# Kernel tuning notes

Measured on AMD Instinct MI355X. Metric: run time of the kernel, lower is better.

## Reference

```python
import jax, jax.numpy as jnp
import numpy as np

N = 50000          # num nodes
E = 1_000_000      # num edges (no self loops by construction)
IN_CH = 128        # in_channels
HEADS = 4
OUT_CH = 16        # out_channels per head
HID = HEADS * OUT_CH  # 64
NEG_SLOPE = 0.2


def setup_inputs() -> dict:
    key = jax.random.key(0)
    k1, k2, k3, k4, k5, k6 = jax.random.split(key, 6)
    x = jax.random.normal(k1, (N, IN_CH), jnp.float32)
    # edges with guaranteed row != col (so add_self_loops == plain concat)
    row = jax.random.randint(k2, (E,), 0, N, dtype=jnp.int32)
    off = jax.random.randint(k3, (E,), 1, N, dtype=jnp.int32)
    col = (row + off) % N
    edge_index = jnp.stack([row, col], axis=0)  # [2, E]
    # xavier-uniform linear weight [HID, IN_CH] (bias=False in module)
    lim_w = float(np.sqrt(6.0 / (IN_CH + HID)))
    W = jax.random.uniform(k4, (HID, IN_CH), jnp.float32, -lim_w, lim_w)
    # xavier-uniform attention vectors [HEADS, OUT_CH]
    lim_a = float(np.sqrt(6.0 / (HEADS + OUT_CH)))
    att_src = jax.random.uniform(k5, (HEADS, OUT_CH), jnp.float32, -lim_a, lim_a)
    att_dst = jax.random.uniform(k6, (HEADS, OUT_CH), jnp.float32, -lim_a, lim_a)
    bias = jnp.zeros((HID,), jnp.float32)
    return {"x": x, "edge_index": edge_index, "W": W,
            "att_src": att_src, "att_dst": att_dst, "bias": bias}


def reference(x, edge_index, W, att_src, att_dst, bias):
    # add self loops (input edges have no self loops, so this matches torch)
    loops = jnp.arange(N, dtype=edge_index.dtype)
    ei = jnp.concatenate([edge_index, jnp.stack([loops, loops], axis=0)], axis=1)
    row, col = ei[0], ei[1]                      # [E+N]
    proj = (x @ W.T).reshape(N, HEADS, OUT_CH)   # [N, H, C]
    src = proj[row]                              # [E+N, H, C] gather
    dst = proj[col]                              # [E+N, H, C] gather
    # MX attention logits per edge per head
    logits = (jnp.einsum('ehc,hc->eh', src, att_src)
              + jnp.einsum('ehc,hc->eh', dst, att_dst))
    logits = jax.nn.leaky_relu(logits, NEG_SLOPE)            # [E+N, H]
    # segment softmax over destination node (all heads at once)
    m = jax.ops.segment_max(logits, col, num_segments=N)    # [N, H]
    e = jnp.exp(logits - m[col])
    s = jax.ops.segment_sum(e, col, num_segments=N)         # [N, H]
    w = e / s[col]                                           # [E+N, H]
    # attention-weighted scatter-add aggregation
    out = jax.ops.segment_sum(src * w[..., None], col, num_segments=N)  # [N, H, C]
    return out.reshape(N, HID) + bias
```

## Files before the change

kernel.cpp:

```cpp
#include <hip/hip_runtime.h>

#define IN_CH   128
#define HEADS   4
#define OUT_CH  16
#define HID     64
#define NEG_SLOPE 0.2f
#define LOG2E   1.44269504088896340736f

#define LDA 136

#define RB      6
#define RSZ     64
#define NRANGE  1024
#define SEG     8192
#define RWIN    2048

typedef __attribute__((ext_vector_type(8))) short short8;
typedef __attribute__((ext_vector_type(4))) float float4v;

__device__ __forceinline__ unsigned short f2bf(float f) {
    unsigned int u = __float_as_uint(f);
    u += 0x7FFFu + ((u >> 16) & 1u);
    return (unsigned short)(u >> 16);
}
__device__ __forceinline__ unsigned int cvt_pk_bf16(float lo, float hi) {
    unsigned int r;
    asm("v_cvt_pk_bf16_f32 %0, %1, %2" : "=v"(r) : "v"(lo), "v"(hi));
    return r;
}
__device__ __forceinline__ void unpack2(unsigned int u, float& lo, float& hi) {
    lo = __uint_as_float(u << 16);
    hi = __uint_as_float(u & 0xffff0000u);
}

__global__ __launch_bounds__(256) void proj_bin_kernel(
    const float* __restrict__ x,
    const float* __restrict__ W,
    const float* __restrict__ att_src,
    const float* __restrict__ att_dst,
    unsigned short* __restrict__ proj,
    float* __restrict__ asrc,
    float* __restrict__ adst,
    const int* __restrict__ src,
    const int* __restrict__ dst,
    int* __restrict__ gcur,
    unsigned int* __restrict__ ebuf,
    int n_nodes, int n_edges, int nblk_proj)
{
    __shared__ __align__(16) char smraw[SEG * 4 + NRANGE * 4];

    const int tid = threadIdx.x;

    if (blockIdx.x >= nblk_proj) {
        unsigned int* eb = (unsigned int*)smraw;
        int*          lc = (int*)(smraw + SEG * 4);

        const int b = blockIdx.x - nblk_proj;
        #pragma unroll
        for (int i = tid; i < NRANGE; i += 256) lc[i] = 0;
        __syncthreads();

        const int e0  = b * SEG;
        const int e1  = min(e0 + SEG, n_edges);
        const int cnt = e1 - e0;

        for (int e = e0 + tid * 4; e < e1; e += 1024) {
            if (e + 4 <= e1) {
                const int4 s4 = *(const int4*)(src + e);
                const int4 d4 = *(const int4*)(dst + e);
                {
                    const int r = d4.x >> RB; atomicAdd(&lc[r], 1);
                    eb[e - e0 + 0] = ((unsigned int)r << 22) | ((unsigned int)(d4.x & (RSZ - 1)) << 16) | (unsigned int)s4.x;
                }
                {
                    const int r = d4.y >> RB; atomicAdd(&lc[r], 1);
                    eb[e - e0 + 1] = ((unsigned int)r << 22) | ((unsigned int)(d4.y & (RSZ - 1)) << 16) | (unsigned int)s4.y;
                }
                {
                    const int r = d4.z >> RB; atomicAdd(&lc[r], 1);
                    eb[e - e0 + 2] = ((unsigned int)r << 22) | ((unsigned int)(d4.z & (RSZ - 1)) << 16) | (unsigned int)s4.z;
                }
                {
                    const int r = d4.w >> RB; atomicAdd(&lc[r], 1);
                    eb[e - e0 + 3] = ((unsigned int)r << 22) | ((unsigned int)(d4.w & (RSZ - 1)) << 16) | (unsigned int)s4.w;
                }
            } else {
                for (int q = e; q < e1; ++q) {
                    const int d = dst[q];
                    const int r = d >> RB;
                    atomicAdd(&lc[r], 1);
                    eb[q - e0] = ((unsigned int)r << 22) | ((unsigned int)(d & (RSZ - 1)) << 16) | (unsigned int)src[q];
                }
            }
        }
        __syncthreads();

        for (int r = tid; r < NRANGE; r += 256) {
            const int c = lc[r];
            if (c) lc[r] = r * RWIN + atomicAdd(&gcur[r], c);
        }
        __syncthreads();

        for (int j = tid; j < cnt; j += 256) {
            const unsigned int p = eb[j];
            const int slot = atomicAdd(&lc[p >> 22], 1);
            ebuf[slot] = p & 0x3FFFFFu;
        }
        return;
    }

    unsigned short* As = (unsigned short*)smraw;
    unsigned short* Bs = (unsigned short*)(smraw + 64 * LDA * 2);

    const int n0 = blockIdx.x * 64;

    #pragma unroll
    for (int i = 0; i < 8; ++i) {
        int idx4 = i * 256 + tid;
        int row  = idx4 >> 5;
        int c4   = (idx4 & 31) * 4;
        float4 v = *(const float4*)(W + row * IN_CH + c4);
        uint2 o;
        o.x = cvt_pk_bf16(v.x, v.y);
        o.y = cvt_pk_bf16(v.z, v.w);
        *(uint2*)(&Bs[row * LDA + c4]) = o;
    }
    #pragma unroll
    for (int i = 0; i < 8; ++i) {
        int idx4 = i * 256 + tid;
        int row  = idx4 >> 5;
        int c4   = (idx4 & 31) * 4;
        int n    = n0 + row;
        float4 v = make_float4(0.f, 0.f, 0.f, 0.f);
        if (n < n_nodes) v = *(const float4*)(x + (size_t)n * IN_CH + c4);
        uint2 o;
        o.x = cvt_pk_bf16(v.x, v.y);
        o.y = cvt_pk_bf16(v.z, v.w);
        *(uint2*)(&As[row * LDA + c4]) = o;
    }
    __syncthreads();

    const int w    = tid >> 6;
    const int lane = tid & 63;
    const int l16  = lane & 15;
    const int quad = lane >> 4;

    float4v acc0 = {0.f,0.f,0.f,0.f};
    float4v acc1 = {0.f,0.f,0.f,0.f};
    float4v acc2 = {0.f,0.f,0.f,0.f};
    float4v acc3 = {0.f,0.f,0.f,0.f};

    const unsigned short* arow = &As[(w * 16 + l16) * LDA + quad * 8];
    const unsigned short* b0   = &Bs[( 0 + l16) * LDA + quad * 8];
    const unsigned short* b1   = &Bs[(16 + l16) * LDA + quad * 8];
    const unsigned short* b2   = &Bs[(32 + l16) * LDA + quad * 8];
    const unsigned short* b3   = &Bs[(48 + l16) * LDA + quad * 8];

    #pragma unroll
    for (int k0 = 0; k0 < IN_CH; k0 += 32) {
        short8 a  = *(const short8*)(arow + k0);
        acc0 = __builtin_amdgcn_mfma_f32_16x16x32_bf16(a, *(const short8*)(b0 + k0), acc0, 0, 0, 0);
        acc1 = __builtin_amdgcn_mfma_f32_16x16x32_bf16(a, *(const short8*)(b1 + k0), acc1, 0, 0, 0);
        acc2 = __builtin_amdgcn_mfma_f32_16x16x32_bf16(a, *(const short8*)(b2 + k0), acc2, 0, 0, 0);
        acc3 = __builtin_amdgcn_mfma_f32_16x16x32_bf16(a, *(const short8*)(b3 + k0), acc3, 0, 0, 0);
    }

    const float as0 = att_src[ 0 + l16], ad0 = att_dst[ 0 + l16];
    const float as1 = att_src[16 + l16], ad1 = att_dst[16 + l16];
    const float as2 = att_src[32 + l16], ad2 = att_dst[32 + l16];
    const float as3 = att_src[48 + l16], ad3 = att_dst[48 + l16];

    #pragma unroll
    for (int r = 0; r < 4; ++r) {
        const int n = n0 + w * 16 + quad * 4 + r;
        const bool ok = (n < n_nodes);
        float v0 = acc0[r], v1 = acc1[r], v2 = acc2[r], v3 = acc3[r];
        if (ok) {
            proj[(size_t)n * HID +  0 + l16] = f2bf(v0);
            proj[(size_t)n * HID + 16 + l16] = f2bf(v1);
            proj[(size_t)n * HID + 32 + l16] = f2bf(v2);
            proj[(size_t)n * HID + 48 + l16] = f2bf(v3);
        }
        float s0 = v0 * as0, s1 = v1 * as1, s2 = v2 * as2, s3 = v3 * as3;
        float d0 = v0 * ad0, d1 = v1 * ad1, d2 = v2 * ad2, d3 = v3 * ad3;
        #pragma unroll
        for (int off = 8; off >= 1; off >>= 1) {
            s0 += __shfl_down(s0, off, 16);
            s1 += __shfl_down(s1, off, 16);
            s2 += __shfl_down(s2, off, 16);
            s3 += __shfl_down(s3, off, 16);
            d0 += __shfl_down(d0, off, 16);
            d1 += __shfl_down(d1, off, 16);
            d2 += __shfl_down(d2, off, 16);
            d3 += __shfl_down(d3, off, 16);
        }
        if (ok && l16 == 0) {
            asrc[n * HEADS + 0] = s0 * LOG2E;
            asrc[n * HEADS + 1] = s1 * LOG2E;
            asrc[n * HEADS + 2] = s2 * LOG2E;
            asrc[n * HEADS + 3] = s3 * LOG2E;
            adst[n * HEADS + 0] = d0 * LOG2E;
            adst[n * HEADS + 1] = d1 * LOG2E;
            adst[n * HEADS + 2] = d2 * LOG2E;
            adst[n * HEADS + 3] = d3 * LOG2E;
        }
    }
}

__global__ __launch_bounds__(512) void gather_kernel(
    const unsigned short* __restrict__ proj,
    const float* __restrict__ asrc,
    const float* __restrict__ adst,
    const int* __restrict__ gcur,
    const unsigned int* __restrict__ ebuf,
    const float* __restrict__ bias,
    float* __restrict__ out,
    int n_nodes)
{
    __shared__ unsigned short csr_s[RWIN + 128];
    __shared__ int hist[RSZ];
    __shared__ int stt[RSZ];
    __shared__ int cur[RSZ];

    const int r    = blockIdx.x;
    const int base = r * RSZ;
    const int tid  = threadIdx.x;

    if (tid < RSZ) hist[tid] = 0;
    __syncthreads();

    const int total = min(gcur[r], RWIN);
    const int s0 = r * RWIN;

    unsigned int ev0 = 0, ev1 = 0, ev2 = 0, ev3 = 0;
    const int j0 = tid, j1 = tid + 512, j2 = tid + 1024, j3 = tid + 1536;
    if (j0 < total) { ev0 = ebuf[s0 + j0]; atomicAdd(&hist[ev0 >> 16], 1); }
    if (j1 < total) { ev1 = ebuf[s0 + j1]; atomicAdd(&hist[ev1 >> 16], 1); }
    if (j2 < total) { ev2 = ebuf[s0 + j2]; atomicAdd(&hist[ev2 >> 16], 1); }
    if (j3 < total) { ev3 = ebuf[s0 + j3]; atomicAdd(&hist[ev3 >> 16], 1); }
    __syncthreads();

    if (tid < RSZ) {
        const int hv = hist[tid];
        int hc = hv;
        #pragma unroll
        for (int o = 1; o < 64; o <<= 1) {
            int u = __shfl_up(hc, o);
            if (tid >= o) hc += u;
        }
        stt[tid] = hc - hv;
        cur[tid] = hc - hv;
    }
    __syncthreads();

    if (j0 < total) { const int sl = atomicAdd(&cur[ev0 >> 16], 1); csr_s[sl] = (unsigned short)ev0; }
    if (j1 < total) { const int sl = atomicAdd(&cur[ev1 >> 16], 1); csr_s[sl] = (unsigned short)ev1; }
    if (j2 < total) { const int sl = atomicAdd(&cur[ev2 >> 16], 1); csr_s[sl] = (unsigned short)ev2; }
    if (j3 < total) { const int sl = atomicAdd(&cur[ev3 >> 16], 1); csr_s[sl] = (unsigned short)ev3; }
    __syncthreads();

    const int l  = tid & 63;
    const int w  = tid >> 6;
    const int il = l & 7;
    const int g  = l >> 3;
    const int h  = il >> 1;
    const int ch = il * 8;

    const int nd = w * 8 + g;
    int n = base + nd;
    const bool nok = (n < n_nodes);
    if (!nok) n = 0;

    const float  ad  = adst[n * HEADS + h];
    const float4 bv0 = *(const float4*)(bias + ch);
    const float4 bv1 = *(const float4*)(bias + ch + 4);

    float zs = asrc[n * HEADS + h] + ad;
    zs = fmaxf(zs, NEG_SLOPE * zs);
    float s = exp2f(zs);
    float a0, a1, a2, a3, a4, a5, a6, a7;
    {
        const uint4 ps = *(const uint4*)(proj + (size_t)n * HID + ch);
        float p0, p1, p2, p3, p4, p5, p6, p7;
        unpack2(ps.x, p0, p1); unpack2(ps.y, p2, p3);
        unpack2(ps.z, p4, p5); unpack2(ps.w, p6, p7);
        a0 = s * p0; a1 = s * p1; a2 = s * p2; a3 = s * p3;
        a4 = s * p4; a5 = s * p5; a6 = s * p6; a7 = s * p7;
    }

    const int st  = stt[nd];
    const int deg = nok ? hist[nd] : 0;

    int m = deg;
    m = max(m, __shfl_xor(m, 8));
    m = max(m, __shfl_xor(m, 16));
    m = max(m, __shfl_xor(m, 32));
    const int kmax = __builtin_amdgcn_readfirstlane(m);

    #define STEP(K)                                                           \
    {                                                                         \
        const bool act = (K) < deg;                                           \
        int sid = (int)csr_s[st + (K)];       \
        sid = act ? sid : 0;                  \
        const uint4 pv = *(const uint4*)(proj + (size_t)sid * HID + ch);      \
        float av = asrc[sid * HEADS + h] + ad;                                \
        av = fmaxf(av, NEG_SLOPE * av);                                       \
        float e = exp2f(av);                                                  \
        e = act ? e : 0.f;                                                    \
        s += e;                                                               \
        float p0, p1, p2, p3, p4, p5, p6, p7;                                 \
        unpack2(pv.x, p0, p1); unpack2(pv.y, p2, p3);                         \
        unpack2(pv.z, p4, p5); unpack2(pv.w, p6, p7);                         \
        a0 = fmaf(e, p0, a0); a1 = fmaf(e, p1, a1);                           \
        a2 = fmaf(e, p2, a2); a3 = fmaf(e, p3, a3);                           \
        a4 = fmaf(e, p4, a4); a5 = fmaf(e, p5, a5);                           \
        a6 = fmaf(e, p6, a6); a7 = fmaf(e, p7, a7);                           \
    }

    for (int k = 0; k < kmax; k += 4) {
        STEP(k);
        STEP(k + 1);
        STEP(k + 2);
        STEP(k + 3);
    }
    #undef STEP

    if (nok) {
        const float inv = 1.0f / s;
        float4 o0, o1;
        o0.x = a0 * inv + bv0.x;
        o0.y = a1 * inv + bv0.y;
        o0.z = a2 * inv + bv0.z;
        o0.w = a3 * inv + bv0.w;
        o1.x = a4 * inv + bv1.x;
        o1.y = a5 * inv + bv1.y;
        o1.z = a6 * inv + bv1.z;
        o1.w = a7 * inv + bv1.w;
        *(float4*)(out + (size_t)n * HID + ch)     = o0;
        *(float4*)(out + (size_t)n * HID + ch + 4) = o1;
    }
}

static inline size_t align16(size_t o) { return (o + 15) & ~(size_t)15; }

extern "C" void kernel_launch(void* const* d_in, const int* in_sizes, int n_in,
                              void* d_out, int out_size, void* d_ws, size_t ws_size,
                              hipStream_t stream)
{
    const float* x       = (const float*)d_in[0];
    const int*   ei      = (const int*)d_in[1];
    const float* W       = (const float*)d_in[2];
    const float* att_src = (const float*)d_in[3];
    const float* att_dst = (const float*)d_in[4];
    const float* bias    = (const float*)d_in[5];
    float* out           = (float*)d_out;

    const int n_nodes = in_sizes[0] / IN_CH;
    const int n_edges = in_sizes[1] / 2;
    const int nproj   = (n_nodes + 63) / 64;
    const int nbin    = (n_edges + SEG - 1) / SEG;
    const int nrange  = (n_nodes + RSZ - 1) / RSZ;

    const int* src = ei;
    const int* dst = ei + n_edges;

    char* base = (char*)d_ws;
    size_t o = 0;
    unsigned short* proj = (unsigned short*)(base + o); o = align16(o + (size_t)n_nodes * HID * 2);
    float* asrc      = (float*)(base + o); o = align16(o + (size_t)n_nodes * HEADS * 4);
    float* adst      = (float*)(base + o); o = align16(o + (size_t)n_nodes * HEADS * 4);
    unsigned int* ebuf = (unsigned int*)(base + o); o = align16(o + (size_t)nrange * RWIN * 4);
    int*   gcur      = (int*)(base + o);   o = align16(o + (size_t)NRANGE * 4);

    hipMemsetAsync(gcur, 0, (size_t)NRANGE * 4, stream);

    proj_bin_kernel<<<nproj + nbin, 256, 0, stream>>>(
        x, W, att_src, att_dst, proj, asrc, adst,
        src, dst, gcur, ebuf, n_nodes, n_edges, nproj);

    gather_kernel<<<nrange, 512, 0, stream>>>(
        proj, asrc, adst, gcur, ebuf, bias, out, n_nodes);
}
```

Before: 131.8 us.

## Precompute edge attention weights in LDS and sort nodes by degree across waves

The gather kernel now computes the per-edge exp2 attention weight for all four heads in a separate block-wide pass into shared memory, so the main loop loads one float instead of fetching asrc and evaluating the exponent. It also caches adst for the range in LDS and uses a 64-lane bitonic sort on degree to permute node-to-wave assignment, grouping similar-degree nodes so each wave's loop trip count (max degree) wastes fewer lanes. The cost is more LDS (32-bit CSR plus the weight array), an extra barrier pass, and a lower per-range edge cap (ECAP 1664 instead of RWIN 2048), which could drop edges if a range ever exceeds the cap.

New measurement: 123.3 us. 1.07x faster.

```diff
diff --git a/kernel.cpp b/kernel.cpp
--- a/kernel.cpp
+++ b/kernel.cpp
@@ -14,6 +14,8 @@
 #define NRANGE  1024
 #define SEG     8192
 #define RWIN    2048
+#define ECAP    1664
+#define EPAD    (ECAP + 128)
 
 typedef __attribute__((ext_vector_type(8))) short short8;
 typedef __attribute__((ext_vector_type(4))) float float4v;
@@ -217,19 +219,26 @@
     float* __restrict__ out,
     int n_nodes)
 {
-    __shared__ unsigned short csr_s[RWIN + 128];
+    __shared__ unsigned int csr_u[EPAD];
+    __shared__ float e_s[EPAD * HEADS];
+    __shared__ float adst_s[RSZ * HEADS];
     __shared__ int hist[RSZ];
     __shared__ int stt[RSZ];
     __shared__ int cur[RSZ];
+    __shared__ int perm[RSZ];
 
     const int r    = blockIdx.x;
     const int base = r * RSZ;
     const int tid  = threadIdx.x;
 
     if (tid < RSZ) hist[tid] = 0;
-    __syncthreads();
-
-    const int total = min(gcur[r], RWIN);
+    if (tid < RSZ * HEADS) {
+        const int nd = tid >> 2;
+        adst_s[tid] = (base + nd < n_nodes) ? adst[(base + nd) * HEADS + (tid & 3)] : 0.f;
+    }
+    __syncthreads();
+
+    const int total = min(gcur[r], ECAP);
     const int s0 = r * RWIN;
 
     unsigned int ev0 = 0, ev1 = 0, ev2 = 0, ev3 = 0;
@@ -250,13 +259,35 @@
         }
         stt[tid] = hc - hv;
         cur[tid] = hc - hv;
-    }
-    __syncthreads();
-
-    if (j0 < total) { const int sl = atomicAdd(&cur[ev0 >> 16], 1); csr_s[sl] = (unsigned short)ev0; }
-    if (j1 < total) { const int sl = atomicAdd(&cur[ev1 >> 16], 1); csr_s[sl] = (unsigned short)ev1; }
-    if (j2 < total) { const int sl = atomicAdd(&cur[ev2 >> 16], 1); csr_s[sl] = (unsigned short)ev2; }
-    if (j3 < total) { const int sl = atomicAdd(&cur[ev3 >> 16], 1); csr_s[sl] = (unsigned short)ev3; }
+        int key = (hv << 6) | tid;
+        #pragma unroll
+        for (int k = 2; k <= 64; k <<= 1) {
+            #pragma unroll
+            for (int j = k >> 1; j > 0; j >>= 1) {
+                const int pk = __shfl_xor(key, j);
+                const bool keepMin = ((tid & j) == 0) == ((tid & k) == 0);
+                key = keepMin ? min(key, pk) : max(key, pk);
+            }
+        }
+        perm[tid] = key & 63;
+    }
+    __syncthreads();
+
+    if (j0 < total) { const int sl = atomicAdd(&cur[ev0 >> 16], 1); csr_u[sl] = ev0; }
+    if (j1 < total) { const int sl = atomicAdd(&cur[ev1 >> 16], 1); csr_u[sl] = ev1; }
+    if (j2 < total) { const int sl = atomicAdd(&cur[ev2 >> 16], 1); csr_u[sl] = ev2; }
+    if (j3 < total) { const int sl = atomicAdd(&cur[ev3 >> 16], 1); csr_u[sl] = ev3; }
+    __syncthreads();
+
+    const int tq = total * HEADS;
+    for (int idx = tid; idx < tq; idx += 512) {
+        const unsigned int u = csr_u[idx >> 2];
+        const int hh  = idx & 3;
+        const int sid = (int)(u & 0xffffu);
+        float av = asrc[sid * HEADS + hh] + adst_s[((u >> 16) << 2) + hh];
+        av = fmaxf(av, NEG_SLOPE * av);
+        e_s[idx] = exp2f(av);
+    }
     __syncthreads();
 
     const int l  = tid & 63;
@@ -266,16 +297,15 @@
     const int h  = il >> 1;
     const int ch = il * 8;
 
-    const int nd = w * 8 + g;
+    const int nd = perm[w * 8 + g];
     int n = base + nd;
     const bool nok = (n < n_nodes);
     if (!nok) n = 0;
 
-    const float  ad  = adst[n * HEADS + h];
     const float4 bv0 = *(const float4*)(bias + ch);
     const float4 bv1 = *(const float4*)(bias + ch + 4);
 
-    float zs = asrc[n * HEADS + h] + ad;
+    float zs = asrc[n * HEADS + h] + adst_s[nd * HEADS + h];
     zs = fmaxf(zs, NEG_SLOPE * zs);
     float s = exp2f(zs);
     float a0, a1, a2, a3, a4, a5, a6, a7;
@@ -300,12 +330,10 @@
     #define STEP(K)                                                           \
     {                                                                         \
         const bool act = (K) < deg;                                           \
-        int sid = (int)csr_s[st + (K)];       \
-        sid = act ? sid : 0;                  \
+        const unsigned int u = csr_u[st + (K)];  \
+        int sid = act ? (int)(u & 0xffffu) : 0;    \
         const uint4 pv = *(const uint4*)(proj + (size_t)sid * HID + ch);      \
-        float av = asrc[sid * HEADS + h] + ad;                                \
-        av = fmaxf(av, NEG_SLOPE * av);                                       \
-        float e = exp2f(av);                                                  \
+        float e = e_s[(st + (K)) * HEADS + h];                                \
         e = act ? e : 0.f;                                                    \
         s += e;                                                               \
         float p0, p1, p2, p3, p4, p5, p6, p7;                                 \
```
